# Optimization experiments

Hardware: AMD Instinct MI355X
Metric: run time of the kernel (lower is better)

## Reference

```python
import jax, jax.numpy as jnp
import numpy as np


def _ln(x, w, b):
    m = x.mean(-1, keepdims=True)
    v = ((x - m) ** 2).mean(-1, keepdims=True)
    return (x - m) * jax.lax.rsqrt(v + 1e-5) * w + b


def _l2n(x):
    return x / jnp.clip(jnp.linalg.norm(x, axis=-1, keepdims=True), 1e-12, None)


def _forward(tokens, emb, ln1_w, ln1_b, wq, wkv, wo, wo_b, knn_scale,
             ln2_w, ln2_b, ff_w1, ff_b1, ff_w2, ff_b2, lnf_w, lnf_b,
             w_logits, b_logits, xl_mems, db_kv, knn_layer, topk):
    B, N = tokens.shape
    depth = wq.shape[0]
    H = knn_scale.shape[0]
    Dh = wkv.shape[-1] // 2
    XL = xl_mems.shape[2]
    NEG = jnp.finfo(emb.dtype).max
    x = emb[tokens]  # [B,N,dim]
    # causal mask with XL-cache offset: triu(j - i + 1)
    causal = jnp.triu(jnp.ones((N, N + XL), bool), XL + 1)
    for l in range(depth):
        h = _ln(x, ln1_w[l], ln1_b[l])
        q = (h @ wq[l]).reshape(B, N, H, Dh).transpose(0, 2, 1, 3)  # [B,H,N,Dh]
        kv = h @ wkv[l]
        k, v = kv[..., :Dh], kv[..., Dh:]  # single shared kv head [B,N,Dh]
        is_knn = (l == knn_layer)
        if is_knn:
            q, k = _l2n(q), _l2n(k)
            scale = jnp.exp(knn_scale)[None, :, None, None]
        else:
            q = q * (Dh ** -0.5)
            scale = 1.0
        k = jnp.concatenate((xl_mems[l, :, :, 0], k), axis=1)  # [B,N+XL,Dh]
        v = jnp.concatenate((xl_mems[l, :, :, 1], v), axis=1)
        sim = jnp.einsum('bhid,bjd->bhij', q, k) * scale
        sim = jnp.where(causal, -NEG, sim)
        if is_knn:
            dbk = _l2n(db_kv[..., 0, :])  # [B,M,Dh] stored keys are l2-normalized
            dbv = db_kv[..., 1, :]
            simdb = jnp.einsum('bhid,bmd->bhim', q, dbk)
            _, idx = jax.lax.top_k(simdb, topk)  # [B,H,N,topk] inner-product KNN
            mem_k = jax.vmap(lambda t, i: t[i])(dbk, idx)  # [B,H,N,topk,Dh]
            mem_v = jax.vmap(lambda t, i: t[i])(dbv, idx)
            sim_mem = jnp.einsum('bhid,bhijd->bhij', q, mem_k) * scale
            attn = jax.nn.softmax(jnp.concatenate((sim_mem, sim), axis=-1), axis=-1)
            mem_attn, loc_attn = attn[..., :topk], attn[..., topk:]
            out = (jnp.einsum('bhij,bjd->bhid', loc_attn, v)
                   + jnp.einsum('bhij,bhijd->bhid', mem_attn, mem_v))
        else:
            attn = jax.nn.softmax(sim, axis=-1)
            out = jnp.einsum('bhij,bjd->bhid', attn, v)
        out = out.transpose(0, 2, 1, 3).reshape(B, N, H * Dh)
        x = out @ wo[l] + wo_b[l] + x
        h = _ln(x, ln2_w[l], ln2_b[l])
        x = jax.nn.gelu(h @ ff_w1[l] + ff_b1[l], approximate=False) @ ff_w2[l] + ff_b2[l] + x
    return _ln(x, lnf_w, lnf_b) @ w_logits + b_logits


def setup_inputs() -> dict:
    B, N, DIM, H, DH, DEPTH, V, XL, M = 2, 1024, 1024, 16, 64, 4, 32000, 256, 4096
    key = jax.random.key(0)
    ks = jax.random.split(key, 12)
    s = 0.02
    rn = lambda k, sh: (jax.random.normal(k, sh) * s).astype(jnp.float32)
    return dict(
        tokens=jax.random.randint(ks[0], (B, N), 0, V, dtype=jnp.int32),
        emb=rn(ks[1], (V, DIM)),
        ln1_w=jnp.ones((DEPTH, DIM), jnp.float32), ln1_b=jnp.zeros((DEPTH, DIM), jnp.float32),
        wq=rn(ks[2], (DEPTH, DIM, H * DH)),
        wkv=rn(ks[3], (DEPTH, DIM, 2 * DH)),
        wo=rn(ks[4], (DEPTH, H * DH, DIM)), wo_b=jnp.zeros((DEPTH, DIM), jnp.float32),
        knn_scale=jnp.full((H,), float(np.log(20.0)), jnp.float32),
        ln2_w=jnp.ones((DEPTH, DIM), jnp.float32), ln2_b=jnp.zeros((DEPTH, DIM), jnp.float32),
        ff_w1=rn(ks[5], (DEPTH, DIM, 4 * DIM)), ff_b1=jnp.zeros((DEPTH, 4 * DIM), jnp.float32),
        ff_w2=rn(ks[6], (DEPTH, 4 * DIM, DIM)), ff_b2=jnp.zeros((DEPTH, DIM), jnp.float32),
        lnf_w=jnp.ones((DIM,), jnp.float32), lnf_b=jnp.zeros((DIM,), jnp.float32),
        w_logits=rn(ks[7], (DIM, V)), b_logits=jnp.zeros((V,), jnp.float32),
        xl_mems=jax.random.normal(ks[8], (DEPTH, B, XL, 2, DH), jnp.float32),
        db_kv=jax.random.normal(ks[9], (B, M, 2, DH), jnp.float32),
        knn_layer=2, topk=32,
    )


def reference(tokens, emb, ln1_w, ln1_b, wq, wkv, wo, wo_b, knn_scale,
              ln2_w, ln2_b, ff_w1, ff_b1, ff_w2, ff_b2, lnf_w, lnf_b,
              w_logits, b_logits, xl_mems, db_kv, knn_layer, topk):
    return _forward(tokens, emb, ln1_w, ln1_b, wq, wkv, wo, wo_b, knn_scale,
                    ln2_w, ln2_b, ff_w1, ff_b1, ff_w2, ff_b2, lnf_w, lnf_b,
                    w_logits, b_logits, xl_mems, db_kv, knn_layer, topk)
```

## Files before the change

kernel.cpp:

```cpp
#include <hip/hip_runtime.h>
#include <hip/hip_bf16.h>
#include <math.h>

#define BB 2
#define NSEQ 1024
#define DIM 1024
#define NH 16
#define DH 64
#define DEPTH 4
#define VOCAB 32000
#define XLM 256
#define MDB 4096
#define TOPK 32
#define KNN_LAYER 2
#define BNROWS (BB * NSEQ)
#define LOGITS_CHUNK 6400
#define NKEYS 1280
#define KSP_PS ((size_t)BB * NKEYS * DH)

typedef __bf16 bf16x8v __attribute__((ext_vector_type(8)));
typedef float f32x4v __attribute__((ext_vector_type(4)));
typedef unsigned short u16x8v __attribute__((ext_vector_type(8)));

__device__ __forceinline__ float bfbits2f(unsigned short u) {
    union { float f; unsigned int i; } v; v.i = ((unsigned int)u) << 16; return v.f;
}
__device__ __forceinline__ unsigned short f2bfbits(float f) {
    union { __hip_bfloat16 b; unsigned short u; } v;
    v.b = __float2bfloat16(f);
    return v.u;
}
__device__ __forceinline__ float bf2f(__hip_bfloat16 h) { return __bfloat162float(h); }
__device__ __forceinline__ __hip_bfloat16 f2bf(float f) { return __float2bfloat16(f); }

__device__ __forceinline__ void gload16(const void* gp, void* lp) {
    __builtin_amdgcn_global_load_lds(
        (const __attribute__((address_space(1))) unsigned int*)gp,
        (__attribute__((address_space(3))) unsigned int*)lp, 16, 0, 0);
}

__global__ __launch_bounds__(256) void embed_kernel(const int* __restrict__ tok,
                                                    const float* __restrict__ emb,
                                                    float* __restrict__ x) {
    int r = blockIdx.x, t = threadIdx.x;
    int id = tok[r];
    const float* er = emb + (size_t)id * DIM;
    float* xr = x + (size_t)r * DIM;
#pragma unroll
    for (int i = 0; i < 4; i++) xr[t + 256 * i] = er[t + 256 * i];
}

__global__ __launch_bounds__(256) void ln_kernel(const float* __restrict__ x,
                                                 const float* __restrict__ w,
                                                 const float* __restrict__ b,
                                                 __hip_bfloat16* __restrict__ y,
                                                 size_t ypS) {
    __shared__ float red[256];
    int r = blockIdx.x, t = threadIdx.x;
    const float* xr = x + (size_t)r * DIM;
    float v[4];
#pragma unroll
    for (int i = 0; i < 4; i++) v[i] = xr[t + 256 * i];
    float s = v[0] + v[1] + v[2] + v[3];
    red[t] = s; __syncthreads();
    for (int st = 128; st; st >>= 1) { if (t < st) red[t] += red[t + st]; __syncthreads(); }
    float mean = red[0] * (1.0f / DIM);
    __syncthreads();
    float s2 = 0.f;
#pragma unroll
    for (int i = 0; i < 4; i++) { float d = v[i] - mean; s2 += d * d; }
    red[t] = s2; __syncthreads();
    for (int st = 128; st; st >>= 1) { if (t < st) red[t] += red[t + st]; __syncthreads(); }
    float rs = rsqrtf(red[0] * (1.0f / DIM) + 1e-5f);
    __hip_bfloat16* yr = y + (size_t)r * DIM;
#pragma unroll
    for (int i = 0; i < 4; i++) {
        int c = t + 256 * i;
        float val = (v[i] - mean) * rs * w[c] + b[c];
        __hip_bfloat16 hv = f2bf(val);
        yr[c] = hv;
        yr[c + ypS] = f2bf(val - bf2f(hv));
    }
}

template <int NP>
__global__ __launch_bounds__(256) void combine_ln(const float* __restrict__ pbuf, size_t pS,
                                                  const float* __restrict__ bias,
                                                  float* __restrict__ x,
                                                  const float* __restrict__ w,
                                                  const float* __restrict__ b,
                                                  __hip_bfloat16* __restrict__ y,
                                                  size_t ypS) {
    __shared__ float red[256];
    int r = blockIdx.x, t = threadIdx.x;
    float v[4];
#pragma unroll
    for (int i = 0; i < 4; i++) {
        int c = t + 256 * i;
        size_t idx = (size_t)r * DIM + c;
        float s = bias[c] + x[idx];
#pragma unroll
        for (int z = 0; z < NP; z++) s += pbuf[(size_t)z * pS + idx];
        v[i] = s;
        x[idx] = s;
    }
    float s = v[0] + v[1] + v[2] + v[3];
    red[t] = s; __syncthreads();
    for (int st = 128; st; st >>= 1) { if (t < st) red[t] += red[t + st]; __syncthreads(); }
    float mean = red[0] * (1.0f / DIM);
    __syncthreads();
    float s2 = 0.f;
#pragma unroll
    for (int i = 0; i < 4; i++) { float d = v[i] - mean; s2 += d * d; }
    red[t] = s2; __syncthreads();
    for (int st = 128; st; st >>= 1) { if (t < st) red[t] += red[t + st]; __syncthreads(); }
    float rs = rsqrtf(red[0] * (1.0f / DIM) + 1e-5f);
    __hip_bfloat16* yr = y + (size_t)r * DIM;
#pragma unroll
    for (int i = 0; i < 4; i++) {
        int c = t + 256 * i;
        float val = (v[i] - mean) * rs * w[c] + b[c];
        __hip_bfloat16 hv = f2bf(val);
        yr[c] = hv;
        yr[c + ypS] = f2bf(val - bf2f(hv));
    }
}

__global__ void l2split_q(float* __restrict__ qf, unsigned short* __restrict__ qs,
                          size_t pS) {
    int r = blockIdx.x, t = threadIdx.x;
    size_t idx = (size_t)r * DH + t;
    float v = qf[idx];
    float s = v * v;
#pragma unroll
    for (int off = 32; off; off >>= 1) s += __shfl_xor(s, off, 64);
    float n = fmaxf(sqrtf(s), 1e-12f);
    v /= n;
    qf[idx] = v;
    unsigned short hv = f2bfbits(v);
    qs[idx] = hv;
    qs[idx + pS] = f2bfbits(v - bfbits2f(hv));
}

__global__ void dbnorm_kernel(const float* __restrict__ db, float* __restrict__ dbkn) {
    int r = blockIdx.x, t = threadIdx.x;
    float v = db[((size_t)r * 2 + 0) * DH + t];
    float s = v * v;
#pragma unroll
    for (int off = 32; off; off >>= 1) s += __shfl_xor(s, off, 64);
    float n = fmaxf(sqrtf(s), 1e-12f);
    dbkn[(size_t)r * DH + t] = v / n;
}

__global__ __launch_bounds__(256) void split_conv(const float* __restrict__ x,
                                                  unsigned short* __restrict__ y,
                                                  size_t pS, size_t n4) {
    size_t idx = (size_t)blockIdx.x * 256 + threadIdx.x;
    if (idx >= n4) return;
    float4 v = *(const float4*)&x[idx * 4];
    float vv[4] = {v.x, v.y, v.z, v.w};
    ushort4 h4, l4;
    unsigned short* hp = (unsigned short*)&h4;
    unsigned short* lp = (unsigned short*)&l4;
#pragma unroll
    for (int j = 0; j < 4; j++) {
        hp[j] = f2bfbits(vv[j]);
        lp[j] = f2bfbits(vv[j] - bfbits2f(hp[j]));
    }
    *(ushort4*)&y[idx * 4] = h4;
    *(ushort4*)&y[idx * 4 + pS] = l4;
}

template <int NP>
__global__ __launch_bounds__(256) void combine_k(const float* __restrict__ pbuf, size_t pS,
                                                 float* __restrict__ out,
                                                 const float* __restrict__ bias,
                                                 const float* __restrict__ res,
                                                 int N, size_t n4) {
    size_t idx = (size_t)blockIdx.x * 256 + threadIdx.x;
    if (idx >= n4) return;
    f32x4v s = *(const f32x4v*)&pbuf[idx * 4];
#pragma unroll
    for (int z = 1; z < NP; z++) {
        f32x4v v = *(const f32x4v*)&pbuf[(size_t)z * pS + idx * 4];
        s += v;
    }
    if (bias) {
        int col = (int)((idx * 4) % (size_t)N);
        const f32x4v bv = *(const f32x4v*)&bias[col];
        s += bv;
    }
    if (res) {
        f32x4v r = *(const f32x4v*)&res[idx * 4];
        s += r;
    }
    *(f32x4v*)&out[idx * 4] = s;
}

template <int NP>
__global__ __launch_bounds__(256) void combine_gelu_split(const float* __restrict__ pbuf, size_t pS,
                                                          const float* __restrict__ bias, int N,
                                                          unsigned short* __restrict__ y, size_t ypS,
                                                          size_t n4) {
    size_t idx = (size_t)blockIdx.x * 256 + threadIdx.x;
    if (idx >= n4) return;
    f32x4v s = *(const f32x4v*)&pbuf[idx * 4];
#pragma unroll
    for (int z = 1; z < NP; z++) {
        f32x4v v = *(const f32x4v*)&pbuf[(size_t)z * pS + idx * 4];
        s += v;
    }
    int col = (int)((idx * 4) % (size_t)N);
    const f32x4v bv = *(const f32x4v*)&bias[col];
    s += bv;
    ushort4 h4, l4;
    unsigned short* hp = (unsigned short*)&h4;
    unsigned short* lp = (unsigned short*)&l4;
#pragma unroll
    for (int j = 0; j < 4; j++) {
        float v = s[j];
        v = 0.5f * v * (1.0f + erff(v * 0.70710678118654752f));
        hp[j] = f2bfbits(v);
        lp[j] = f2bfbits(v - bfbits2f(hp[j]));
    }
    *(ushort4*)&y[idx * 4] = h4;
    *(ushort4*)&y[idx * 4 + ypS] = l4;
}

template <int NORM>
__global__ void kv_prep(const float* __restrict__ kvf, const float* __restrict__ xlm,
                        unsigned short* __restrict__ ksp, unsigned short* __restrict__ vtp) {
    int key = blockIdx.x, b = blockIdx.y, d = threadIdx.x;
    float kvv, vvv;
    if (key < XLM) {
        kvv = xlm[(((size_t)b * XLM + key) * 2 + 0) * DH + d];
        vvv = xlm[(((size_t)b * XLM + key) * 2 + 1) * DH + d];
    } else {
        const float* r = &kvf[(size_t)(b * NSEQ + key - XLM) * 128];
        kvv = r[d]; vvv = r[64 + d];
        if (NORM) {
            float s = kvv * kvv;
#pragma unroll
            for (int off = 32; off; off >>= 1) s += __shfl_xor(s, off, 64);
            kvv /= fmaxf(sqrtf(s), 1e-12f);
        }
    }
    unsigned short kh = f2bfbits(kvv), kl = f2bfbits(kvv - bfbits2f(kh));
    unsigned short vh = f2bfbits(vvv), vl = f2bfbits(vvv - bfbits2f(vh));
    size_t ko = (size_t)b * NKEYS * DH + (size_t)key * DH + d;
    ksp[ko] = kh; ksp[ko + KSP_PS] = kl;
    size_t vo = (size_t)b * DH * NKEYS + (size_t)d * NKEYS + key;
    vtp[vo] = vh; vtp[vo + KSP_PS] = vl;
}

__global__ __launch_bounds__(256) void wconv(const float* __restrict__ W,
                                             __hip_bfloat16* __restrict__ WT,
                                             size_t wpS, int K, int N, int ldw,
                                             int wlo) {
    __shared__ float tile[64][65];
    int k0 = blockIdx.x * 64, n0 = blockIdx.y * 64;
    int t = threadIdx.x;
    int r = t >> 4, c4 = (t & 15) * 4;
#pragma unroll
    for (int rr = 0; rr < 4; rr++) {
        int row = rr * 16 + r;
        float4 v = *(const float4*)&W[(size_t)(k0 + row) * ldw + n0 + c4];
        tile[row][c4] = v.x; tile[row][c4 + 1] = v.y; tile[row][c4 + 2] = v.z; tile[row][c4 + 3] = v.w;
    }
    __syncthreads();
#pragma unroll
    for (int rr = 0; rr < 4; rr++) {
        int nrow = rr * 16 + r;
        size_t base = (size_t)(n0 + nrow) * K + k0 + c4;
#pragma unroll
        for (int j = 0; j < 4; j++) {
            float val = tile[c4 + j][nrow];
            __hip_bfloat16 hv = f2bf(val);
            WT[base + j] = hv;
            if (wlo) WT[base + j + wpS] = f2bf(val - bf2f(hv));
        }
    }
}

template <typename OT, int ACT, int TERMS, int MODE>
__global__ __launch_bounds__(256) void gemm_split(const __hip_bfloat16* __restrict__ A, int lda, size_t apS,
                                                  const __hip_bfloat16* __restrict__ BT, int ldb, size_t bpS,
                                                  OT* __restrict__ C, int ldc, size_t cpS, int K,
                                                  const float* __restrict__ bias,
                                                  const float* __restrict__ res,
                                                  int bh0) {
    __shared__ __align__(16) __hip_bfloat16 sAh[128 * 32];
    __shared__ __align__(16) __hip_bfloat16 sBh[128 * 32];
    __shared__ __align__(16) __hip_bfloat16 sAl[TERMS >= 2 ? 128 * 32 : 1];
    __shared__ __align__(16) __hip_bfloat16 sBl[TERMS >= 3 ? 128 * 32 : 1];
    if constexpr (MODE == 1) {
        int bh = bh0 + blockIdx.z;
        A += ((size_t)(bh >> 4) * NSEQ) * lda + (bh & 15) * DH;
        BT += (size_t)(bh >> 4) * MDB * ldb;
        C += (size_t)blockIdx.z * NSEQ * ldc;
    }
    if constexpr (MODE == 2) {
        A += (size_t)blockIdx.z * K;
        BT += (size_t)blockIdx.z * K;
        C += (size_t)blockIdx.z * cpS;
    }
    int bn = blockIdx.x * 128;
    int bm = blockIdx.y * 128;
    int t = threadIdx.x;
    int lane = t & 63, wid = t >> 6;
    int wr = wid >> 1, wc = wid & 1;
    int lr = lane & 15, kc = lane >> 4;

    f32x4v acc[4][4];
#pragma unroll
    for (int m = 0; m < 4; m++)
#pragma unroll
        for (int n = 0; n < 4; n++) acc[m][n] = (f32x4v){0.f, 0.f, 0.f, 0.f};

    for (int k0 = 0; k0 < K; k0 += 32) {
        __syncthreads();
#pragma unroll
        for (int it = 0; it < 2; it++) {
            int e = wid * 128 + it * 64 + lane;
            int r = e >> 2;
            int cl = (e & 3) ^ ((r >> 1) & 3);
            size_t aoff = (size_t)(bm + r) * lda + k0 + cl * 8;
            size_t boff = (size_t)(bn + r) * ldb + k0 + cl * 8;
            int dst = (wid * 128 + it * 64) * 8;
            gload16(&A[aoff], &sAh[dst]);
            gload16(&BT[boff], &sBh[dst]);
            if constexpr (TERMS >= 2) gload16(&A[aoff + apS], &sAl[dst]);
            if constexpr (TERMS >= 3) gload16(&BT[boff + bpS], &sBl[dst]);
        }
        __syncthreads();

        bf16x8v ah[4], al[4], bh[4], bl[4];
#pragma unroll
        for (int m = 0; m < 4; m++) {
            int row = wr * 64 + m * 16 + lr;
            int off = row * 32 + ((kc ^ ((row >> 1) & 3)) << 3);
            ah[m] = *(const bf16x8v*)&sAh[off];
            if constexpr (TERMS >= 2) al[m] = *(const bf16x8v*)&sAl[off];
        }
#pragma unroll
        for (int n = 0; n < 4; n++) {
            int row = wc * 64 + n * 16 + lr;
            int off = row * 32 + ((kc ^ ((row >> 1) & 3)) << 3);
            bh[n] = *(const bf16x8v*)&sBh[off];
            if constexpr (TERMS >= 3) bl[n] = *(const bf16x8v*)&sBl[off];
        }
#pragma unroll
        for (int m = 0; m < 4; m++)
#pragma unroll
            for (int n = 0; n < 4; n++) {
                acc[m][n] = __builtin_amdgcn_mfma_f32_16x16x32_bf16(ah[m], bh[n], acc[m][n], 0, 0, 0);
                if constexpr (TERMS >= 2)
                    acc[m][n] = __builtin_amdgcn_mfma_f32_16x16x32_bf16(al[m], bh[n], acc[m][n], 0, 0, 0);
                if constexpr (TERMS >= 3)
                    acc[m][n] = __builtin_amdgcn_mfma_f32_16x16x32_bf16(ah[m], bl[n], acc[m][n], 0, 0, 0);
            }
    }

#pragma unroll
    for (int m = 0; m < 4; m++) {
#pragma unroll
        for (int n = 0; n < 4; n++) {
            int gcol = bn + wc * 64 + n * 16 + lr;
            float bv = bias ? bias[gcol] : 0.f;
#pragma unroll
            for (int j = 0; j < 4; j++) {
                int grow = bm + wr * 64 + m * 16 + kc * 4 + j;
                float v = acc[m][n][j] + bv;
                if (ACT == 1) v = 0.5f * v * (1.0f + erff(v * 0.70710678118654752f));
                if (res) v += res[(size_t)grow * ldc + gcol];
                size_t idx = (size_t)grow * ldc + gcol;
                if constexpr (__is_same(OT, float)) {
                    C[idx] = v;
                } else if constexpr (__is_same(OT, unsigned short)) {
                    C[idx] = f2bfbits(v);
                } else {
                    __hip_bfloat16 hv = f2bf(v);
                    C[idx] = hv;
                    C[idx + cpS] = f2bf(v - bf2f(hv));
                }
            }
        }
    }
}

template <int KNNL>
__global__ __launch_bounds__(256) void flash_kernel(const float* __restrict__ q,
                                                    const unsigned short* __restrict__ ksp,
                                                    const unsigned short* __restrict__ vtp,
                                                    const float* __restrict__ knn_scale,
                                                    __hip_bfloat16* __restrict__ out,
                                                    size_t opS,
                                                    float* __restrict__ stats) {
    __shared__ __align__(16) unsigned short sKh[64 * 64];
    __shared__ __align__(16) unsigned short sKl[64 * 64];
    __shared__ __align__(16) unsigned short sVh[64 * 64];
    __shared__ __align__(16) unsigned short sVl[64 * 64];
    __shared__ __align__(16) float sPf[4 * 16 * 64];

    int qt = blockIdx.x, h = blockIdx.y, b = blockIdx.z;
    int q0 = qt * 64;
    int t = threadIdx.x;
    int w = t >> 6;
    int lane = t & 63;
    int lr = lane & 15, kc = lane >> 4;
    int wbase = w * 1024;

    float scale = KNNL ? __expf(knn_scale[h]) : 0.125f;

    bf16x8v qh[2], ql[2];
    {
        const float* qbase = q + (size_t)(b * NSEQ + q0 + w * 16 + lr) * DIM + h * DH;
#pragma unroll
        for (int ks = 0; ks < 2; ks++) {
            const float* s = qbase + ks * 32 + kc * 8;
            float4 a = *(const float4*)s;
            float4 c2 = *(const float4*)(s + 4);
            float vv[8] = {a.x, a.y, a.z, a.w, c2.x, c2.y, c2.z, c2.w};
            u16x8v hi, lo;
#pragma unroll
            for (int j = 0; j < 8; j++) {
                hi[j] = f2bfbits(vv[j]);
                lo[j] = f2bfbits(vv[j] - bfbits2f(hi[j]));
            }
            qh[ks] = *(bf16x8v*)&hi;
            ql[ks] = *(bf16x8v*)&lo;
        }
    }

    float m[4], l[4];
    f32x4v o[4];
#pragma unroll
    for (int j = 0; j < 4; j++) { m[j] = -1e30f; l[j] = 0.f; }
#pragma unroll
    for (int f = 0; f < 4; f++) o[f] = (f32x4v){0.f, 0.f, 0.f, 0.f};

    int ntiles = 5 + qt;
    size_t kbase = (size_t)b * NKEYS * DH;
    size_t vbase = (size_t)b * DH * NKEYS;

    for (int T = 0; T < ntiles; T++) {
        __syncthreads();
#pragma unroll
        for (int i2 = 0; i2 < 2; i2++) {
            int cbase = i2 * 256 + w * 64;
            int c = cbase + lane;
            int key = c >> 3, ch = (c & 7) ^ (key & 7);
            size_t ko = kbase + (size_t)(T * 64 + key) * DH + ch * 8;
            gload16(&ksp[ko], &sKh[cbase * 8]);
            gload16(&ksp[ko + KSP_PS], &sKl[cbase * 8]);
            int dim = c >> 3, k8 = (c & 7) ^ (dim & 7);
            size_t vo = vbase + (size_t)dim * NKEYS + T * 64 + k8 * 8;
            gload16(&vtp[vo], &sVh[cbase * 8]);
            gload16(&vtp[vo + KSP_PS], &sVl[cbase * 8]);
        }
        __syncthreads();

        f32x4v s4[4];
#pragma unroll
        for (int n = 0; n < 4; n++) s4[n] = (f32x4v){0.f, 0.f, 0.f, 0.f};
#pragma unroll
        for (int ks = 0; ks < 2; ks++) {
            bf16x8v qh_ = qh[ks], ql_ = ql[ks];
#pragma unroll
            for (int n = 0; n < 4; n++) {
                int row = n * 16 + lr;
                int off = row * 64 + (((ks * 4 + kc) ^ (lr & 7)) << 3);
                bf16x8v kh = *(const bf16x8v*)&sKh[off];
                bf16x8v kl = *(const bf16x8v*)&sKl[off];
                s4[n] = __builtin_amdgcn_mfma_f32_16x16x32_bf16(qh_, kh, s4[n], 0, 0, 0);
                s4[n] = __builtin_amdgcn_mfma_f32_16x16x32_bf16(ql_, kh, s4[n], 0, 0, 0);
                s4[n] = __builtin_amdgcn_mfma_f32_16x16x32_bf16(qh_, kl, s4[n], 0, 0, 0);
            }
        }

#pragma unroll
        for (int n = 0; n < 4; n++) {
            int key = T * 64 + n * 16 + lr;
#pragma unroll
            for (int j = 0; j < 4; j++) {
                int gq = q0 + w * 16 + kc * 4 + j;
                float sv = s4[n][j] * scale;
                s4[n][j] = (key <= XLM + gq) ? sv : -1e30f;
            }
        }

        float tm[4];
#pragma unroll
        for (int j = 0; j < 4; j++) {
            float v = fmaxf(fmaxf(s4[0][j], s4[1][j]), fmaxf(s4[2][j], s4[3][j]));
            v = fmaxf(v, __shfl_xor(v, 1, 64));
            v = fmaxf(v, __shfl_xor(v, 2, 64));
            v = fmaxf(v, __shfl_xor(v, 4, 64));
            v = fmaxf(v, __shfl_xor(v, 8, 64));
            tm[j] = v;
        }
        float alpha[4];
#pragma unroll
        for (int j = 0; j < 4; j++) {
            float mnew = fmaxf(m[j], tm[j]);
            alpha[j] = __expf(m[j] - mnew);
            m[j] = mnew;
        }
        float psum[4] = {0.f, 0.f, 0.f, 0.f};
#pragma unroll
        for (int n = 0; n < 4; n++)
#pragma unroll
            for (int j = 0; j < 4; j++) {
                float p = __expf(s4[n][j] - m[j]);
                s4[n][j] = p;
                psum[j] += p;
            }
#pragma unroll
        for (int j = 0; j < 4; j++) {
            float v = psum[j];
            v += __shfl_xor(v, 1, 64);
            v += __shfl_xor(v, 2, 64);
            v += __shfl_xor(v, 4, 64);
            v += __shfl_xor(v, 8, 64);
            l[j] = l[j] * alpha[j] + v;
        }
#pragma unroll
        for (int f = 0; f < 4; f++)
#pragma unroll
            for (int j = 0; j < 4; j++) o[f][j] *= alpha[j];

#pragma unroll
        for (int n = 0; n < 4; n++) {
            int chunkcol = 2 * n + (lr >> 3);
#pragma unroll
            for (int j = 0; j < 4; j++) {
                int row = kc * 4 + j;
                int off = wbase + row * 64 + (((chunkcol ^ (row & 7)) << 3) + (lr & 7));
                sPf[off] = s4[n][j];
            }
        }

#pragma unroll
        for (int ks = 0; ks < 2; ks++) {
            int poff = wbase + lr * 64 + (((ks * 4 + kc) ^ (lr & 7)) << 3);
            float4 a = *(const float4*)&sPf[poff];
            float4 c2 = *(const float4*)&sPf[poff + 4];
            float vv[8] = {a.x, a.y, a.z, a.w, c2.x, c2.y, c2.z, c2.w};
            u16x8v hib, lob;
#pragma unroll
            for (int j = 0; j < 8; j++) {
                hib[j] = f2bfbits(vv[j]);
                lob[j] = f2bfbits(vv[j] - bfbits2f(hib[j]));
            }
            bf16x8v ph = *(bf16x8v*)&hib;
            bf16x8v pl = *(bf16x8v*)&lob;
#pragma unroll
            for (int f = 0; f < 4; f++) {
                int row = f * 16 + lr;
                int off = row * 64 + (((ks * 4 + kc) ^ (lr & 7)) << 3);
                bf16x8v vh = *(const bf16x8v*)&sVh[off];
                bf16x8v vl = *(const bf16x8v*)&sVl[off];
                o[f] = __builtin_amdgcn_mfma_f32_16x16x32_bf16(ph, vh, o[f], 0, 0, 0);
                o[f] = __builtin_amdgcn_mfma_f32_16x16x32_bf16(pl, vh, o[f], 0, 0, 0);
                o[f] = __builtin_amdgcn_mfma_f32_16x16x32_bf16(ph, vl, o[f], 0, 0, 0);
            }
        }
    }

    float inv[4];
#pragma unroll
    for (int j = 0; j < 4; j++) inv[j] = 1.0f / l[j];
    unsigned short* outu = (unsigned short*)out;
#pragma unroll
    for (int f = 0; f < 4; f++)
#pragma unroll
        for (int j = 0; j < 4; j++) {
            int gq = q0 + w * 16 + kc * 4 + j;
            size_t oidx = (size_t)(b * NSEQ + gq) * DIM + h * DH + f * 16 + lr;
            float v = o[f][j] * inv[j];
            unsigned short hv = f2bfbits(v);
            outu[oidx] = hv;
            outu[oidx + opS] = f2bfbits(v - bfbits2f(hv));
        }
    if (KNNL && lr == 0) {
#pragma unroll
        for (int j = 0; j < 4; j++) {
            int gq = q0 + w * 16 + kc * 4 + j;
            size_t srow = (((size_t)b * NH + h) * NSEQ + gq) * 2;
            stats[srow] = m[j];
            stats[srow + 1] = l[j];
        }
    }
}

__global__ __launch_bounds__(256) void knn_select(const unsigned short* __restrict__ simdb,
                                                  const float* __restrict__ db,
                                                  const float* __restrict__ qf,
                                                  const float* __restrict__ dbkn,
                                                  const float* __restrict__ knn_scale,
                                                  const float* __restrict__ stats,
                                                  __hip_bfloat16* __restrict__ out,
                                                  size_t opS,
                                                  int bh0) {
    __shared__ unsigned short sv[4 * 4096];

    int bh = bh0 + blockIdx.y;
    int b = bh >> 4, h = bh & 15;
    int t = threadIdx.x;
    int w = t >> 6, lane = t & 63;
    int i = blockIdx.x * 4 + w;
    unsigned short* svw = &sv[w * 4096];

    const unsigned short* srow = &simdb[((size_t)blockIdx.y * NSEQ + i) * MDB];
#pragma unroll
    for (int it = 0; it < 8; it++) {
        int g = it * 64 + lane;
        int c = g >> 3, sub = g & 7;
        u16x8v d = *(const u16x8v*)&srow[(size_t)g * 8];
        *(u16x8v*)&svw[c * 64 + ((sub ^ (c & 7)) << 3)] = d;
    }

    float lmax = -1e30f; int lidx = 0;
#pragma unroll
    for (int c = 0; c < 64; c++) {
        float v = bfbits2f(svw[c * 64 + (lane ^ ((c & 7) << 3))]);
        if (v > lmax) { lmax = v; lidx = c * 64 + lane; }
    }

    int tidx = 0;
    for (int it = 0; it < TOPK; it++) {
        float v = lmax; int idx = lidx;
#pragma unroll
        for (int off = 32; off; off >>= 1) {
            float v2 = __shfl_xor(v, off, 64);
            int i2 = __shfl_xor(idx, off, 64);
            if (v2 > v || (v2 == v && i2 < idx)) { v = v2; idx = i2; }
        }
        if (lane == it) tidx = idx;
        int col = idx & 63, cc = idx >> 6;
        if (lane == 0) svw[cc * 64 + (col ^ ((cc & 7) << 3))] = 0xFF80;
        float rv = bfbits2f(svw[lane * 64 + (col ^ ((lane & 7) << 3))]);
        int ridx = lane * 64 + col;
#pragma unroll
        for (int off = 32; off; off >>= 1) {
            float v2 = __shfl_xor(rv, off, 64);
            int i2 = __shfl_xor(ridx, off, 64);
            if (v2 > rv || (v2 == rv && i2 < ridx)) { rv = v2; ridx = i2; }
        }
        if (lane == col) { lmax = rv; lidx = ridx; }
    }

    float srec = -1e30f;
    if (lane < TOPK) {
        const float* qrow = &qf[(size_t)(b * NSEQ + i) * DIM + h * DH];
        const float* krow = &dbkn[((size_t)b * MDB + tidx) * DH];
        float s = 0.f;
#pragma unroll
        for (int d4 = 0; d4 < 16; d4++) {
            float4 a = *(const float4*)&qrow[d4 * 4];
            float4 k2 = *(const float4*)&krow[d4 * 4];
            s += a.x * k2.x + a.y * k2.y + a.z * k2.z + a.w * k2.w;
        }
        srec = s;
    }

    float scl = __expf(knn_scale[h]);
    size_t srow_idx = (((size_t)b * NH + h) * NSEQ + i) * 2;
    float m_loc = stats[srow_idx], l_loc = stats[srow_idx + 1];
    float mm = srec;
#pragma unroll
    for (int off = 32; off; off >>= 1) mm = fmaxf(mm, __shfl_xor(mm, off, 64));
    float M = fmaxf(m_loc, mm * scl);
    float co = __expf(m_loc - M);
    float e = (lane < TOPK) ? __expf(srec * scl - M) : 0.f;
    float esum = e;
#pragma unroll
    for (int off = 32; off; off >>= 1) esum += __shfl_xor(esum, off, 64);
    float denom = l_loc * co + esum;

    float acc = 0.f;
#pragma unroll
    for (int j = 0; j < TOPK; j++) {
        int idxj = __shfl(tidx, j, 64);
        float ej = __shfl(e, j, 64);
        acc += ej * db[(((size_t)b * MDB + idxj) * 2 + 1) * DH + lane];
    }

    size_t op = (size_t)(b * NSEQ + i) * DIM + h * DH + lane;
    float o_loc = bf2f(out[op]) + bf2f(out[op + opS]);
    float nv = (o_loc * l_loc * co + acc) / denom;
    __hip_bfloat16 hv = f2bf(nv);
    out[op] = hv;
    out[op + opS] = f2bf(nv - bf2f(hv));
}

extern "C" void kernel_launch(void* const* d_in, const int* in_sizes, int n_in,
                              void* d_out, int out_size, void* d_ws, size_t ws_size,
                              hipStream_t stream) {
    const int* tokens = (const int*)d_in[0];
    const float* emb = (const float*)d_in[1];
    const float* ln1_w = (const float*)d_in[2];
    const float* ln1_b = (const float*)d_in[3];
    const float* wq = (const float*)d_in[4];
    const float* wkv = (const float*)d_in[5];
    const float* wo = (const float*)d_in[6];
    const float* wo_b = (const float*)d_in[7];
    const float* knn_scale = (const float*)d_in[8];
    const float* ln2_w = (const float*)d_in[9];
    const float* ln2_b = (const float*)d_in[10];
    const float* ff_w1 = (const float*)d_in[11];
    const float* ff_b1 = (const float*)d_in[12];
    const float* ff_w2 = (const float*)d_in[13];
    const float* ff_b2 = (const float*)d_in[14];
    const float* lnf_w = (const float*)d_in[15];
    const float* lnf_b = (const float*)d_in[16];
    const float* w_logits = (const float*)d_in[17];
    const float* b_logits = (const float*)d_in[18];
    const float* xl_mems = (const float*)d_in[19];
    const float* db_kv = (const float*)d_in[20];

    const size_t PS_H = (size_t)BNROWS * DIM;
    char* p = (char*)d_ws;
    float* x = (float*)p;                p += PS_H * 4;
    __hip_bfloat16* hb = (__hip_bfloat16*)p;  p += PS_H * 2 * 2;
    float* qf = (float*)p;               p += PS_H * 4;
    float* kvf = (float*)p;              p += (size_t)BNROWS * 128 * 4;
    float* dbkn = (float*)p;             p += (size_t)BB * MDB * DH * 4;
    float* stats = (float*)p;            p += (size_t)BB * NH * NSEQ * 2 * 4;
    unsigned short* ksp = (unsigned short*)p; p += KSP_PS * 2 * 2;
    unsigned short* vtp = (unsigned short*)p; p += KSP_PS * 2 * 2;
    __hip_bfloat16* wT = (__hip_bfloat16*)p; p += (size_t)4096 * DIM * 2 * 2;

    unsigned short* qsplit = (unsigned short*)wT;
    unsigned short* dbks = (unsigned short*)wT + 2 * PS_H;
    const size_t PS_DB = (size_t)BB * MDB * DH;

    const size_t PS_MID = (size_t)BNROWS * 4 * DIM;
    __hip_bfloat16* midb = (__hip_bfloat16*)d_out;
    float* logits = (float*)d_out;
    float* part = (float*)((char*)d_out + ((size_t)96 << 20));

    embed_kernel<<<BNROWS, 256, 0, stream>>>(tokens, emb, x);
    dbnorm_kernel<<<BB * MDB, 64, 0, stream>>>(db_kv, dbkn);
    ln_kernel<<<BNROWS, 256, 0, stream>>>(x, ln1_w, ln1_b, hb, PS_H);

    for (int l = 0; l < DEPTH; l++) {
        const float* wq_l = wq + (size_t)l * DIM * DIM;
        const float* wkv_l = wkv + (size_t)l * DIM * 128;
        const float* wo_l = wo + (size_t)l * DIM * DIM;
        const float* xlm_l = xl_mems + (size_t)l * BB * XLM * 2 * DH;

        wconv<<<dim3(16, 16), 256, 0, stream>>>(wq_l, wT, (size_t)DIM * DIM, DIM, DIM, DIM, 1);
        gemm_split<float, 0, 3, 2><<<dim3(DIM / 128, BNROWS / 128, 4), 256, 0, stream>>>(
            hb, DIM, PS_H, wT, DIM, (size_t)DIM * DIM, part, DIM, PS_H, 256, nullptr, nullptr, 0);
        combine_k<4><<<(PS_H / 4 + 255) / 256, 256, 0, stream>>>(
            part, PS_H, qf, nullptr, nullptr, DIM, PS_H / 4);
        wconv<<<dim3(16, 2), 256, 0, stream>>>(wkv_l, wT, (size_t)128 * DIM, DIM, 128, 128, 1);
        gemm_split<float, 0, 3, 2><<<dim3(1, BNROWS / 128, 16), 256, 0, stream>>>(
            hb, DIM, PS_H, wT, DIM, (size_t)128 * DIM, part, 128, (size_t)BNROWS * 128, 64, nullptr, nullptr, 0);
        combine_k<16><<<((size_t)BNROWS * 128 / 4 + 255) / 256, 256, 0, stream>>>(
            part, (size_t)BNROWS * 128, kvf, nullptr, nullptr, 128, (size_t)BNROWS * 128 / 4);

        if (l == KNN_LAYER) {
            l2split_q<<<BNROWS * NH, 64, 0, stream>>>(qf, qsplit, PS_H);
            kv_prep<1><<<dim3(NKEYS, BB), 64, 0, stream>>>(kvf, xlm_l, ksp, vtp);
            split_conv<<<(PS_DB / 4 + 255) / 256, 256, 0, stream>>>(dbkn, dbks, PS_DB, PS_DB / 4);
            flash_kernel<1><<<dim3(NSEQ / 64, NH, BB), 256, 0, stream>>>(
                qf, ksp, vtp, knn_scale, hb, PS_H, stats);
            const int CHUNK = 8;
            for (int bh0 = 0; bh0 < BB * NH; bh0 += CHUNK) {
                gemm_split<unsigned short, 0, 1, 1><<<dim3(MDB / 128, NSEQ / 128, CHUNK), 256, 0, stream>>>(
                    (const __hip_bfloat16*)qsplit, DIM, PS_H,
                    (const __hip_bfloat16*)dbks, DH, PS_DB,
                    (unsigned short*)d_out, MDB, 0, DH, nullptr, nullptr, bh0);
                knn_select<<<dim3(NSEQ / 4, CHUNK), 256, 0, stream>>>(
                    (const unsigned short*)d_out, db_kv, qf, dbkn, knn_scale, stats, hb, PS_H, bh0);
            }
        } else {
            kv_prep<0><<<dim3(NKEYS, BB), 64, 0, stream>>>(kvf, xlm_l, ksp, vtp);
            flash_kernel<0><<<dim3(NSEQ / 64, NH, BB), 256, 0, stream>>>(
                qf, ksp, vtp, knn_scale, hb, PS_H, stats);
        }

        wconv<<<dim3(16, 16), 256, 0, stream>>>(wo_l, wT, (size_t)DIM * DIM, DIM, DIM, DIM, 1);
        gemm_split<float, 0, 3, 2><<<dim3(DIM / 128, BNROWS / 128, 4), 256, 0, stream>>>(
            hb, DIM, PS_H, wT, DIM, (size_t)DIM * DIM, part, DIM, PS_H, 256, nullptr, nullptr, 0);
        combine_ln<4><<<BNROWS, 256, 0, stream>>>(
            part, PS_H, wo_b + (size_t)l * DIM, x,
            ln2_w + (size_t)l * DIM, ln2_b + (size_t)l * DIM, hb, PS_H);

        wconv<<<dim3(16, 64), 256, 0, stream>>>(ff_w1 + (size_t)l * DIM * 4 * DIM, wT, (size_t)4096 * DIM, DIM, 4 * DIM, 4 * DIM, 1);
        gemm_split<float, 0, 3, 2><<<dim3(4 * DIM / 128, BNROWS / 128, 2), 256, 0, stream>>>(
            hb, DIM, PS_H, wT, DIM, (size_t)4096 * DIM, part, 4 * DIM, PS_MID, 512, nullptr, nullptr, 0);
        combine_gelu_split<2><<<(PS_MID / 4 + 255) / 256, 256, 0, stream>>>(
            part, PS_MID, ff_b1 + (size_t)l * 4 * DIM, 4 * DIM,
            (unsigned short*)midb, PS_MID, PS_MID / 4);

        wconv<<<dim3(64, 16), 256, 0, stream>>>(ff_w2 + (size_t)l * 4 * DIM * DIM, wT, (size_t)DIM * 4096, 4 * DIM, DIM, DIM, 1);
        gemm_split<float, 0, 3, 2><<<dim3(DIM / 128, BNROWS / 128, 4), 256, 0, stream>>>(
            midb, 4 * DIM, PS_MID, wT, 4 * DIM, (size_t)DIM * 4096, part, DIM, PS_H, 1024, nullptr, nullptr, 0);
        const float* nw = (l < DEPTH - 1) ? ln1_w + (size_t)(l + 1) * DIM : lnf_w;
        const float* nb = (l < DEPTH - 1) ? ln1_b + (size_t)(l + 1) * DIM : lnf_b;
        combine_ln<4><<<BNROWS, 256, 0, stream>>>(
            part, PS_H, ff_b2 + (size_t)l * DIM, x, nw, nb, hb, PS_H);
    }

    for (int c0 = 0; c0 < VOCAB; c0 += LOGITS_CHUNK) {
        wconv<<<dim3(16, LOGITS_CHUNK / 64), 256, 0, stream>>>(
            w_logits + c0, wT, 0, DIM, LOGITS_CHUNK, VOCAB, 0);
        gemm_split<float, 0, 1, 0><<<dim3(LOGITS_CHUNK / 128, BNROWS / 128), 256, 0, stream>>>(
            hb, DIM, PS_H, wT, DIM, 0, logits + c0, VOCAB, 0, DIM,
            b_logits + c0, nullptr, 0);
    }
}
```

Before: 2.252 ms.

## Fuse Q and KV projections into one GEMM and double-buffer flash K/V tiles

The separate Q and KV projection GEMMs and their combine kernels are merged into one GEMM over a concatenated 1152-column weight, followed by a combine that scatters rows into the q and kv buffers. This removes two launches and the 16-way split-K partial buffer for the narrow KV GEMM. The flash attention kernel now double-buffers its K/V shared-memory tiles, so the next tile's global loads are issued while the current tile is being computed. That doubles K/V LDS use and may lower occupancy.

```diff
diff --git a/kernel.cpp b/kernel.cpp
--- a/kernel.cpp
+++ b/kernel.cpp
@@ -16,6 +16,7 @@
 #define BNROWS (BB * NSEQ)
 #define LOGITS_CHUNK 6400
 #define NKEYS 1280
+#define NQKV 1152
 #define KSP_PS ((size_t)BB * NKEYS * DH)
 
 typedef __bf16 bf16x8v __attribute__((ext_vector_type(8)));
@@ -195,6 +196,26 @@
         s += r;
     }
     *(f32x4v*)&out[idx * 4] = s;
+}
+
+template <int NP>
+__global__ __launch_bounds__(256) void combine_qkv(const float* __restrict__ pbuf, size_t pS,
+                                                   float* __restrict__ qf,
+                                                   float* __restrict__ kvf,
+                                                   size_t n4) {
+    size_t idx = (size_t)blockIdx.x * 256 + threadIdx.x;
+    if (idx >= n4) return;
+    f32x4v s = *(const f32x4v*)&pbuf[idx * 4];
+#pragma unroll
+    for (int z = 1; z < NP; z++) {
+        f32x4v v = *(const f32x4v*)&pbuf[(size_t)z * pS + idx * 4];
+        s += v;
+    }
+    size_t e = idx * 4;
+    size_t row = e / NQKV;
+    int col = (int)(e - row * NQKV);
+    if (col < DIM) *(f32x4v*)&qf[row * DIM + col] = s;
+    else *(f32x4v*)&kvf[row * 128 + (col - DIM)] = s;
 }
 
 template <int NP>
@@ -396,10 +417,10 @@
                                                     __hip_bfloat16* __restrict__ out,
                                                     size_t opS,
                                                     float* __restrict__ stats) {
-    __shared__ __align__(16) unsigned short sKh[64 * 64];
-    __shared__ __align__(16) unsigned short sKl[64 * 64];
-    __shared__ __align__(16) unsigned short sVh[64 * 64];
-    __shared__ __align__(16) unsigned short sVl[64 * 64];
+    __shared__ __align__(16) unsigned short sKh[2][4096];
+    __shared__ __align__(16) unsigned short sKl[2][4096];
+    __shared__ __align__(16) unsigned short sVh[2][4096];
+    __shared__ __align__(16) unsigned short sVl[2][4096];
     __shared__ __align__(16) float sPf[4 * 16 * 64];
 
     int qt = blockIdx.x, h = blockIdx.y, b = blockIdx.z;
@@ -443,22 +464,28 @@
     size_t kbase = (size_t)b * NKEYS * DH;
     size_t vbase = (size_t)b * DH * NKEYS;
 
-    for (int T = 0; T < ntiles; T++) {
-        __syncthreads();
+    auto stage = [&](int buf, int T) {
 #pragma unroll
         for (int i2 = 0; i2 < 2; i2++) {
             int cbase = i2 * 256 + w * 64;
             int c = cbase + lane;
             int key = c >> 3, ch = (c & 7) ^ (key & 7);
             size_t ko = kbase + (size_t)(T * 64 + key) * DH + ch * 8;
-            gload16(&ksp[ko], &sKh[cbase * 8]);
-            gload16(&ksp[ko + KSP_PS], &sKl[cbase * 8]);
+            gload16(&ksp[ko], &sKh[buf][cbase * 8]);
+            gload16(&ksp[ko + KSP_PS], &sKl[buf][cbase * 8]);
             int dim = c >> 3, k8 = (c & 7) ^ (dim & 7);
             size_t vo = vbase + (size_t)dim * NKEYS + T * 64 + k8 * 8;
-            gload16(&vtp[vo], &sVh[cbase * 8]);
-            gload16(&vtp[vo + KSP_PS], &sVl[cbase * 8]);
-        }
-        __syncthreads();
+            gload16(&vtp[vo], &sVh[buf][cbase * 8]);
+            gload16(&vtp[vo + KSP_PS], &sVl[buf][cbase * 8]);
+        }
+    };
+
+    stage(0, 0);
+    __syncthreads();
+    int cur = 0;
+
+    for (int T = 0; T < ntiles; T++) {
+        if (T + 1 < ntiles) stage(cur ^ 1, T + 1);
 
         f32x4v s4[4];
 #pragma unroll
@@ -470,8 +497,8 @@
             for (int n = 0; n < 4; n++) {
                 int row = n * 16 + lr;
                 int off = row * 64 + (((ks * 4 + kc) ^ (lr & 7)) << 3);
-                bf16x8v kh = *(const bf16x8v*)&sKh[off];
-                bf16x8v kl = *(const bf16x8v*)&sKl[off];
+                bf16x8v kh = *(const bf16x8v*)&sKh[cur][off];
+                bf16x8v kl = *(const bf16x8v*)&sKl[cur][off];
                 s4[n] = __builtin_amdgcn_mfma_f32_16x16x32_bf16(qh_, kh, s4[n], 0, 0, 0);
                 s4[n] = __builtin_amdgcn_mfma_f32_16x16x32_bf16(ql_, kh, s4[n], 0, 0, 0);
                 s4[n] = __builtin_amdgcn_mfma_f32_16x16x32_bf16(qh_, kl, s4[n], 0, 0, 0);
@@ -558,13 +585,16 @@
             for (int f = 0; f < 4; f++) {
                 int row = f * 16 + lr;
                 int off = row * 64 + (((ks * 4 + kc) ^ (lr & 7)) << 3);
-                bf16x8v vh = *(const bf16x8v*)&sVh[off];
-                bf16x8v vl = *(const bf16x8v*)&sVl[off];
+                bf16x8v vh = *(const bf16x8v*)&sVh[cur][off];
+                bf16x8v vl = *(const bf16x8v*)&sVl[cur][off];
                 o[f] = __builtin_amdgcn_mfma_f32_16x16x32_bf16(ph, vh, o[f], 0, 0, 0);
                 o[f] = __builtin_amdgcn_mfma_f32_16x16x32_bf16(pl, vh, o[f], 0, 0, 0);
                 o[f] = __builtin_amdgcn_mfma_f32_16x16x32_bf16(ph, vl, o[f], 0, 0, 0);
             }
         }
+
+        __syncthreads();
+        cur ^= 1;
     }
 
     float inv[4];
@@ -740,6 +770,8 @@
     float* logits = (float*)d_out;
     float* part = (float*)((char*)d_out + ((size_t)96 << 20));
 
+    const size_t PS_QKV = (size_t)BNROWS * NQKV;
+
     embed_kernel<<<BNROWS, 256, 0, stream>>>(tokens, emb, x);
     dbnorm_kernel<<<BB * MDB, 64, 0, stream>>>(db_kv, dbkn);
     ln_kernel<<<BNROWS, 256, 0, stream>>>(x, ln1_w, ln1_b, hb, PS_H);
@@ -750,16 +782,12 @@
         const float* wo_l = wo + (size_t)l * DIM * DIM;
         const float* xlm_l = xl_mems + (size_t)l * BB * XLM * 2 * DH;
 
-        wconv<<<dim3(16, 16), 256, 0, stream>>>(wq_l, wT, (size_t)DIM * DIM, DIM, DIM, DIM, 1);
-        gemm_split<float, 0, 3, 2><<<dim3(DIM / 128, BNROWS / 128, 4), 256, 0, stream>>>(
-            hb, DIM, PS_H, wT, DIM, (size_t)DIM * DIM, part, DIM, PS_H, 256, nullptr, nullptr, 0);
-        combine_k<4><<<(PS_H / 4 + 255) / 256, 256, 0, stream>>>(
-            part, PS_H, qf, nullptr, nullptr, DIM, PS_H / 4);
-        wconv<<<dim3(16, 2), 256, 0, stream>>>(wkv_l, wT, (size_t)128 * DIM, DIM, 128, 128, 1);
-        gemm_split<float, 0, 3, 2><<<dim3(1, BNROWS / 128, 16), 256, 0, stream>>>(
-            hb, DIM, PS_H, wT, DIM, (size_t)128 * DIM, part, 128, (size_t)BNROWS * 128, 64, nullptr, nullptr, 0);
-        combine_k<16><<<((size_t)BNROWS * 128 / 4 + 255) / 256, 256, 0, stream>>>(
-            part, (size_t)BNROWS * 128, kvf, nullptr, nullptr, 128, (size_t)BNROWS * 128 / 4);
+        wconv<<<dim3(16, 16), 256, 0, stream>>>(wq_l, wT, (size_t)NQKV * DIM, DIM, DIM, DIM, 1);
+        wconv<<<dim3(16, 2), 256, 0, stream>>>(wkv_l, wT + (size_t)DIM * DIM, (size_t)NQKV * DIM, DIM, 128, 128, 1);
+        gemm_split<float, 0, 3, 2><<<dim3(NQKV / 128, BNROWS / 128, 4), 256, 0, stream>>>(
+            hb, DIM, PS_H, wT, DIM, (size_t)NQKV * DIM, part, NQKV, PS_QKV, 256, nullptr, nullptr, 0);
+        combine_qkv<4><<<(PS_QKV / 4 + 255) / 256, 256, 0, stream>>>(
+            part, PS_QKV, qf, kvf, PS_QKV / 4);
 
         if (l == KNN_LAYER) {
             l2split_q<<<BNROWS * NH, 64, 0, stream>>>(qf, qsplit, PS_H);
```

After: 2.229 ms. About the same (-1.0%).
